# Performance work log

Measured on AMD Instinct MI355X. Metric: run time of the kernel, lower is better.

Reference implementation:

```python
import jax, jax.numpy as jnp
import numpy as np

DIM = 768
B, S = 16, 1024
EPS = 1e-5


def setup_inputs() -> dict:
    key = jax.random.key(0)
    ks = jax.random.split(key, 13)
    std = 1.0 / np.sqrt(DIM)
    inp = {
        "x_A": jax.random.normal(ks[0], (B, S, DIM), jnp.float32),
        "x_B": jax.random.normal(ks[1], (B, S, DIM), jnp.float32),
        "x_C": jax.random.normal(ks[2], (B, S, DIM), jnp.float32),
        "W_q": jax.random.normal(ks[3], (DIM, DIM), jnp.float32) * std,
        "b_q": jax.random.normal(ks[4], (DIM,), jnp.float32) * std,
        "W_k": jax.random.normal(ks[5], (DIM, DIM), jnp.float32) * std,
        "b_k": jax.random.normal(ks[6], (DIM,), jnp.float32) * std,
        "W_v": jax.random.normal(ks[7], (DIM, DIM), jnp.float32) * std,
        "b_v": jax.random.normal(ks[8], (DIM,), jnp.float32) * std,
        "gamma": jnp.ones((DIM,), jnp.float32),
        "beta": jnp.zeros((DIM,), jnp.float32),
        "W_fc": jax.random.normal(ks[9], (DIM, DIM), jnp.float32) * std,
        "b_fc": jax.random.normal(ks[10], (DIM,), jnp.float32) * std,
    }
    return inp


def _linear(x, W, b):
    # torch nn.Linear: x @ W.T + b
    return jnp.einsum('bsd,ed->bse', x, W) + b


def _layernorm(x, gamma, beta):
    mu = jnp.mean(x, axis=-1, keepdims=True)
    var = jnp.mean((x - mu) ** 2, axis=-1, keepdims=True)
    return (x - mu) * jax.lax.rsqrt(var + EPS) * gamma + beta


def reference(x_A, x_B, x_C, W_q, b_q, W_k, b_k, W_v, b_v, gamma, beta, W_fc, b_fc):
    scale = 1.0 / jnp.sqrt(jnp.float32(DIM))
    Q = _linear(x_C, W_q, b_q)
    K_A = _linear(x_A, W_k, b_k)
    K_B = _linear(x_B, W_k, b_k)
    V_A = _linear(x_A, W_v, b_v)
    V_B = _linear(x_B, W_v, b_v)
    attn_A = jax.nn.softmax(jnp.einsum('bqd,bkd->bqk', Q, K_A) * scale, axis=-1)
    attn_B = jax.nn.softmax(jnp.einsum('bqd,bkd->bqk', Q, K_B) * scale, axis=-1)
    interp_A = jnp.einsum('bqk,bkd->bqd', attn_A, V_A)
    interp_B = jnp.einsum('bqk,bkd->bqd', attn_B, V_B)
    h = _layernorm(interp_A + interp_B + x_C, gamma, beta)
    return _linear(h, W_fc, b_fc)
```

## Files before the change

kernel.cpp:

```cpp
#include <hip/hip_runtime.h>

#define DIMV 768
#define BATCH 16
#define SEQ 1024
#define LN_EPS 1e-5f

typedef __attribute__((ext_vector_type(8))) short bf16x8;
typedef __attribute__((ext_vector_type(4))) float f32x4;
typedef unsigned short ushort_t;

__device__ __forceinline__ unsigned short f2bf(float f) {
    unsigned u = __float_as_uint(f);
    u = (u + 0x7FFFu + ((u >> 16) & 1u)) >> 16;
    return (unsigned short)u;
}

__global__ __launch_bounds__(256) void gemm_bf16_nt(
    const ushort_t* __restrict__ A, const ushort_t* __restrict__ B,
    const float* __restrict__ bias, const float* __restrict__ bias2,
    void* __restrict__ Cout, void* __restrict__ Cout2,
    int K, int lda, int ldb, int ldc, float scale, int mode,
    long long sAz, long long sBz, long long sCz)
{
    int bx = blockIdx.x, by = blockIdx.y, bz = blockIdx.z;
    {
        const unsigned Z  = gridDim.z;
        const unsigned nx = gridDim.x, ny = gridDim.y;
        if (Z > 1) {
            const unsigned nxy = nx * ny;
            const unsigned lid = ((unsigned)bz * ny + (unsigned)by) * nx + (unsigned)bx;
            unsigned r;
            if ((Z & 7u) == 0u) {
                const unsigned c  = lid & 7u;
                const unsigned rp = lid >> 3;
                bz = (int)(c + 8u * (rp / nxy));
                r  = rp % nxy;
            } else {
                bz = (int)(lid % Z);
                r  = lid / Z;
            }
            bx = (int)(r % nx);
            by = (int)(r / nx);
        } else {
            const unsigned nwg = nx * ny;
            if ((nwg & 7u) == 0u) {
                const unsigned lid = (unsigned)by * nx + (unsigned)bx;
                const unsigned nl  = (lid & 7u) * (nwg >> 3) + (lid >> 3);
                bx = (int)(nl % nx);
                by = (int)(nl / nx);
            }
        }
    }

    A += (long long)bz * sAz;
    B += (long long)bz * sBz;
    float*    Cf  = (float*)Cout    + ((mode == 0 || mode == 3) ? (long long)bz * sCz : 0);
    ushort_t* Ch  = (ushort_t*)Cout + ((mode == 1 || mode == 2) ? (long long)bz * sCz : 0);
    ushort_t* Ch2 = (ushort_t*)Cout2;

    __shared__ ushort_t As[3][128 * 32];
    __shared__ ushort_t Bs[3][128 * 32];

    const int t    = threadIdx.x;
    const int wave = t >> 6;
    const int lane = t & 63;
    const int quad = lane >> 4;
    const int lr   = lane & 15;
    const int wy   = wave >> 1;
    const int wx   = wave & 1;

    const int m0 = by * 128;
    const int n0 = bx * 128;

    const ushort_t* Abase = A + (long long)m0 * lda;
    const ushort_t* Bbase = B + (long long)n0 * ldb;

    auto issue = [&](int k0, int slot) {
        #pragma unroll
        for (int i = 0; i < 2; ++i) {
            const int idx = t + 256 * i;
            const int r   = idx >> 2;
            const int q   = idx & 3;
            const int c   = (q ^ ((r >> 1) & 3)) * 8;
            __builtin_amdgcn_global_load_lds(
                (const __attribute__((address_space(1))) unsigned int*)(Abase + (long long)r * lda + k0 + c),
                (__attribute__((address_space(3))) unsigned int*)&As[slot][idx * 8], 16, 0, 0);
            __builtin_amdgcn_global_load_lds(
                (const __attribute__((address_space(1))) unsigned int*)(Bbase + (long long)r * ldb + k0 + c),
                (__attribute__((address_space(3))) unsigned int*)&Bs[slot][idx * 8], 16, 0, 0);
        }
    };

    int offA[4], offB[4];
    #pragma unroll
    for (int i = 0; i < 4; ++i) {
        const int rowA = wy * 64 + i * 16 + lr;
        offA[i] = rowA * 32 + ((quad ^ ((rowA >> 1) & 3)) * 8);
        const int rowB = wx * 64 + i * 16 + lr;
        offB[i] = rowB * 32 + ((quad ^ ((rowB >> 1) & 3)) * 8);
    }

    f32x4 acc[4][4] = {};

    const int NK = K >> 5;
    issue(0, 0);
    int cur = 0, nxt = 1;
    for (int ki = 0; ki < NK; ++ki) {
        const int kn = (ki + 1 < NK) ? (ki + 1) << 5 : 0;
        issue(kn, nxt);
        asm volatile("s_waitcnt vmcnt(4)" ::: "memory");
        asm volatile("s_barrier" ::: "memory");

        const ushort_t* as = &As[cur][0];
        const ushort_t* bs = &Bs[cur][0];
        bf16x8 af[4], bfr[4];
        #pragma unroll
        for (int i = 0; i < 4; ++i) af[i]  = *(const bf16x8*)&as[offA[i]];
        #pragma unroll
        for (int j = 0; j < 4; ++j) bfr[j] = *(const bf16x8*)&bs[offB[j]];

        #pragma unroll
        for (int i = 0; i < 4; ++i)
            #pragma unroll
            for (int j = 0; j < 4; ++j)
                acc[i][j] = __builtin_amdgcn_mfma_f32_16x16x32_bf16(
                    af[i], bfr[j], acc[i][j], 0, 0, 0);

        cur = nxt;
        nxt = (nxt == 2) ? 0 : nxt + 1;
    }

    #pragma unroll
    for (int j = 0; j < 4; ++j) {
        const int n = n0 + wx * 64 + j * 16 + lr;
        float bv;
        if (mode == 4) bv = (n < DIMV) ? bias[n] : bias2[n - DIMV];
        else           bv = bias ? bias[n] : 0.0f;
        #pragma unroll
        for (int i = 0; i < 4; ++i) {
            #pragma unroll
            for (int r = 0; r < 4; ++r) {
                const int m = m0 + wy * 64 + i * 16 + quad * 4 + r;
                const float val = acc[i][j][r] * scale + bv;
                if (mode == 0) {
                    Cf[(long long)m * ldc + n] = val;
                } else if (mode == 3) {
                    Cf[(long long)m * ldc + n] += val;
                } else if (mode == 1) {
                    Ch[(long long)m * ldc + n] = f2bf(val);
                } else if (mode == 2) {
                    const int b = m >> 10, s = m & 1023;
                    Ch[(long long)b * (DIMV * SEQ) + (long long)n * SEQ + s] = f2bf(val);
                } else {
                    if (n < DIMV) {
                        Ch[(long long)m * ldc + n] = f2bf(val);
                    } else {
                        const int b = m >> 10, s = m & 1023;
                        Ch2[(long long)b * (DIMV * SEQ) + (long long)(n - DIMV) * SEQ + s] = f2bf(val);
                    }
                }
            }
        }
    }
}

__global__ __launch_bounds__(256) void f32_to_bf16(
    const float* __restrict__ in, ushort_t* __restrict__ out)
{
    const long long i = ((long long)blockIdx.x * 256 + threadIdx.x) * 4;
    float4 v = *reinterpret_cast<const float4*>(in + i);
    ushort4 o;
    o.x = f2bf(v.x); o.y = f2bf(v.y); o.z = f2bf(v.z); o.w = f2bf(v.w);
    *reinterpret_cast<ushort4*>(out + i) = o;
}

__global__ __launch_bounds__(256) void softmax_inplace(float* __restrict__ S)
{
    float* s = S + (long long)blockIdx.x * SEQ;
    const int t = threadIdx.x;
    __shared__ float red[256];

    float4 v = *reinterpret_cast<const float4*>(&s[t * 4]);
    float mx = fmaxf(fmaxf(v.x, v.y), fmaxf(v.z, v.w));
    red[t] = mx;
    __syncthreads();
    for (int st = 128; st > 0; st >>= 1) {
        if (t < st) red[t] = fmaxf(red[t], red[t + st]);
        __syncthreads();
    }
    mx = red[0];
    __syncthreads();

    v.x = __expf(v.x - mx); v.y = __expf(v.y - mx);
    v.z = __expf(v.z - mx); v.w = __expf(v.w - mx);
    red[t] = v.x + v.y + v.z + v.w;
    __syncthreads();
    for (int st = 128; st > 0; st >>= 1) {
        if (t < st) red[t] += red[t + st];
        __syncthreads();
    }
    const float inv = 1.0f / red[0];

    ushort4 o;
    o.x = f2bf(v.x * inv); o.y = f2bf(v.y * inv);
    o.z = f2bf(v.z * inv); o.w = f2bf(v.w * inv);
    *reinterpret_cast<ushort4*>((ushort_t*)s + t * 4) = o;
}

__global__ __launch_bounds__(256) void add_layernorm(
    const float* __restrict__ ACC, const float* __restrict__ xC,
    const float* __restrict__ gamma, const float* __restrict__ beta,
    ushort_t* __restrict__ H)
{
    const long long row = blockIdx.x;
    const float* a = ACC + row * DIMV;
    const float* x = xC  + row * DIMV;
    ushort_t*    h = H   + row * DIMV;
    const int t = threadIdx.x;

    __shared__ float r1[256];
    __shared__ float r2[256];

    float vals[3];
    float s = 0.f, ss = 0.f;
    #pragma unroll
    for (int i = 0; i < 3; ++i) {
        const int j = t + i * 256;
        float v = a[j] + x[j];
        vals[i] = v;
        s += v; ss += v * v;
    }
    r1[t] = s; r2[t] = ss;
    __syncthreads();
    for (int st = 128; st > 0; st >>= 1) {
        if (t < st) { r1[t] += r1[t + st]; r2[t] += r2[t + st]; }
        __syncthreads();
    }
    const float mu  = r1[0] * (1.0f / DIMV);
    const float var = r2[0] * (1.0f / DIMV) - mu * mu;
    const float inv = rsqrtf(var + LN_EPS);

    #pragma unroll
    for (int i = 0; i < 3; ++i) {
        const int j = t + i * 256;
        h[j] = f2bf((vals[i] - mu) * inv * gamma[j] + beta[j]);
    }
}

extern "C" void kernel_launch(void* const* d_in, const int* in_sizes, int n_in,
                              void* d_out, int out_size, void* d_ws, size_t ws_size,
                              hipStream_t stream)
{
    const float* xA    = (const float*)d_in[0];
    const float* xB    = (const float*)d_in[1];
    const float* xC    = (const float*)d_in[2];
    const float* Wq    = (const float*)d_in[3];
    const float* bq    = (const float*)d_in[4];
    const float* Wk    = (const float*)d_in[5];
    const float* bk    = (const float*)d_in[6];
    const float* Wv    = (const float*)d_in[7];
    const float* bv    = (const float*)d_in[8];
    const float* gamma = (const float*)d_in[9];
    const float* beta  = (const float*)d_in[10];
    const float* Wfc   = (const float*)d_in[11];
    const float* bfc   = (const float*)d_in[12];
    float* out = (float*)d_out;

    const long long eW   = (long long)DIMV * DIMV;
    const long long perB = (long long)SEQ * DIMV;
    const long long perP = (long long)SEQ * SEQ;

    const long long wBytes        = 4 * eW * 2;
    const long long perBatchBytes = 14 * perB + 4 * perP;

    long long Cmax = ((long long)ws_size - wBytes) / perBatchBytes;
    if (Cmax > BATCH) Cmax = BATCH;
    if (Cmax < 1)     Cmax = 1;
    const int nChunks = (int)((BATCH + Cmax - 1) / Cmax);
    const int CbStd   = (BATCH + nChunks - 1) / nChunks;

    char* cur = (char*)d_ws;
    ushort_t* Wqb  = (ushort_t*)cur; cur += eW * 2;
    ushort_t* Wkvb = (ushort_t*)cur; cur += 2 * eW * 2;
    ushort_t* Wfcb = (ushort_t*)cur; cur += eW * 2;
    char* chunkBase = cur;

    const float scale = 0.03608439182435161f;

    f32_to_bf16<<<(int)(eW / 1024), 256, 0, stream>>>(Wq,  Wqb);
    f32_to_bf16<<<(int)(eW / 1024), 256, 0, stream>>>(Wk,  Wkvb);
    f32_to_bf16<<<(int)(eW / 1024), 256, 0, stream>>>(Wv,  Wkvb + eW);
    f32_to_bf16<<<(int)(eW / 1024), 256, 0, stream>>>(Wfc, Wfcb);

    for (int b0 = 0; b0 < BATCH; b0 += CbStd) {
        const int Cb = (b0 + CbStd <= BATCH) ? CbStd : (BATCH - b0);
        const long long off = (long long)b0 * perB;

        char* p = chunkBase;
        ushort_t* xABb = (ushort_t*)p;
        float*    ACC  = (float*)p;    p += (long long)Cb * 4 * perB;
        float*    Sf   = (float*)p;
        ushort_t* xCb  = (ushort_t*)p; p += (long long)Cb * 4 * perP;
        ushort_t* Qb   = (ushort_t*)p; p += (long long)Cb * 2 * perB;
        ushort_t* Kb   = (ushort_t*)p; p += (long long)Cb * 4 * perB;
        ushort_t* Vtb  = (ushort_t*)p; p += (long long)Cb * 4 * perB;

        dim3 gq  (DIMV / 128, Cb * (SEQ / 128), 1);
        dim3 gkv (2 * DIMV / 128, 2 * Cb * (SEQ / 128), 1);
        dim3 gsc (SEQ / 128, SEQ / 128, Cb);
        dim3 gpv (DIMV / 128, SEQ / 128, Cb);
        const int gcv = (int)((long long)Cb * perB / 1024);

        f32_to_bf16<<<gcv, 256, 0, stream>>>(xC + off, xCb);
        gemm_bf16_nt<<<gq, 256, 0, stream>>>(xCb, Wqb, bq, nullptr, Qb, nullptr,
            DIMV, DIMV, DIMV, DIMV, 1.f, 1, 0, 0, 0);
        f32_to_bf16<<<gcv, 256, 0, stream>>>(xA + off, xABb);
        f32_to_bf16<<<gcv, 256, 0, stream>>>(xB + off, xABb + (long long)Cb * perB);
        gemm_bf16_nt<<<gkv, 256, 0, stream>>>(xABb, Wkvb, bk, bv, Kb, Vtb,
            DIMV, DIMV, DIMV, DIMV, 1.f, 4, 0, 0, 0);

        gemm_bf16_nt<<<gsc, 256, 0, stream>>>(Qb, Kb, nullptr, nullptr, Sf, nullptr,
            DIMV, DIMV, DIMV, SEQ, scale, 0, perB, perB, perP);
        softmax_inplace<<<Cb * SEQ, 256, 0, stream>>>(Sf);
        gemm_bf16_nt<<<gpv, 256, 0, stream>>>((const ushort_t*)Sf, Vtb, nullptr, nullptr, ACC, nullptr,
            SEQ, 2 * SEQ, SEQ, DIMV, 1.f, 0, 2 * perP, perB, perB);

        gemm_bf16_nt<<<gsc, 256, 0, stream>>>(Qb, Kb + (long long)Cb * perB, nullptr, nullptr, Sf, nullptr,
            DIMV, DIMV, DIMV, SEQ, scale, 0, perB, perB, perP);
        softmax_inplace<<<Cb * SEQ, 256, 0, stream>>>(Sf);
        gemm_bf16_nt<<<gpv, 256, 0, stream>>>((const ushort_t*)Sf, Vtb + (long long)Cb * perB, nullptr, nullptr, ACC, nullptr,
            SEQ, 2 * SEQ, SEQ, DIMV, 1.f, 3, 2 * perP, perB, perB);

        add_layernorm<<<Cb * SEQ, 256, 0, stream>>>(ACC, xC + off, gamma, beta, Qb);

        gemm_bf16_nt<<<gq, 256, 0, stream>>>(Qb, Wfcb, bfc, nullptr, out + off, nullptr,
            DIMV, DIMV, DIMV, DIMV, 1.f, 0, 0, 0, 0);
    }
}
```

Before: 731.9 us.

## Merge A/B attention into single concatenated-key pass and deepen GEMM prefetch to 4 stages

Lays out K for A and B interleaved per batch (and V transposed with 2*SEQ columns), so one score GEMM computes both Q·K_A and Q·K_B. A single softmax kernel normalises each half separately, and one PV GEMM with K=2048 sums both attention outputs. This removes two launches and the read-modify-write accumulate pass. The GEMM mainloop also moves from a 3-slot, 1-ahead prefetch to a 4-slot, 2-ahead prefetch, which uses more LDS and may lower occupancy. The score buffer doubles, which can reduce how many batches fit in one chunk.

```diff
diff --git a/kernel.cpp b/kernel.cpp
--- a/kernel.cpp
+++ b/kernel.cpp
@@ -20,7 +20,7 @@
     const float* __restrict__ bias, const float* __restrict__ bias2,
     void* __restrict__ Cout, void* __restrict__ Cout2,
     int K, int lda, int ldb, int ldc, float scale, int mode,
-    long long sAz, long long sBz, long long sCz)
+    long long sAz, long long sBz, long long sCz, int CbArg)
 {
     int bx = blockIdx.x, by = blockIdx.y, bz = blockIdx.z;
     {
@@ -54,12 +54,12 @@
 
     A += (long long)bz * sAz;
     B += (long long)bz * sBz;
-    float*    Cf  = (float*)Cout    + ((mode == 0 || mode == 3) ? (long long)bz * sCz : 0);
-    ushort_t* Ch  = (ushort_t*)Cout + ((mode == 1 || mode == 2) ? (long long)bz * sCz : 0);
+    float*    Cf  = (float*)Cout    + ((mode == 0) ? (long long)bz * sCz : 0);
+    ushort_t* Ch  = (ushort_t*)Cout + ((mode == 1) ? (long long)bz * sCz : 0);
     ushort_t* Ch2 = (ushort_t*)Cout2;
 
-    __shared__ ushort_t As[3][128 * 32];
-    __shared__ ushort_t Bs[3][128 * 32];
+    __shared__ ushort_t As[4][128 * 32];
+    __shared__ ushort_t Bs[4][128 * 32];
 
     const int t    = threadIdx.x;
     const int wave = t >> 6;
@@ -104,15 +104,15 @@
 
     const int NK = K >> 5;
     issue(0, 0);
-    int cur = 0, nxt = 1;
+    issue(32, 1);
     for (int ki = 0; ki < NK; ++ki) {
-        const int kn = (ki + 1 < NK) ? (ki + 1) << 5 : 0;
-        issue(kn, nxt);
-        asm volatile("s_waitcnt vmcnt(4)" ::: "memory");
+        const int k2 = (ki + 2 < NK) ? (ki + 2) << 5 : (NK - 1) << 5;
+        issue(k2, (ki + 2) & 3);
+        asm volatile("s_waitcnt vmcnt(8)" ::: "memory");
         asm volatile("s_barrier" ::: "memory");
 
-        const ushort_t* as = &As[cur][0];
-        const ushort_t* bs = &Bs[cur][0];
+        const ushort_t* as = &As[ki & 3][0];
+        const ushort_t* bs = &Bs[ki & 3][0];
         bf16x8 af[4], bfr[4];
         #pragma unroll
         for (int i = 0; i < 4; ++i) af[i]  = *(const bf16x8*)&as[offA[i]];
@@ -125,9 +125,6 @@
             for (int j = 0; j < 4; ++j)
                 acc[i][j] = __builtin_amdgcn_mfma_f32_16x16x32_bf16(
                     af[i], bfr[j], acc[i][j], 0, 0, 0);
-
-        cur = nxt;
-        nxt = (nxt == 2) ? 0 : nxt + 1;
     }
 
     #pragma unroll
@@ -144,19 +141,16 @@
                 const float val = acc[i][j][r] * scale + bv;
                 if (mode == 0) {
                     Cf[(long long)m * ldc + n] = val;
-                } else if (mode == 3) {
-                    Cf[(long long)m * ldc + n] += val;
                 } else if (mode == 1) {
                     Ch[(long long)m * ldc + n] = f2bf(val);
-                } else if (mode == 2) {
-                    const int b = m >> 10, s = m & 1023;
-                    Ch[(long long)b * (DIMV * SEQ) + (long long)n * SEQ + s] = f2bf(val);
                 } else {
+                    const int bh = m >> 10, s = m & 1023;
+                    const int hf = (bh >= CbArg) ? 1 : 0;
+                    const int b  = bh - (hf ? CbArg : 0);
                     if (n < DIMV) {
-                        Ch[(long long)m * ldc + n] = f2bf(val);
+                        Ch[(long long)b * (2 * SEQ * DIMV) + (long long)(hf * SEQ + s) * DIMV + n] = f2bf(val);
                     } else {
-                        const int b = m >> 10, s = m & 1023;
-                        Ch2[(long long)b * (DIMV * SEQ) + (long long)(n - DIMV) * SEQ + s] = f2bf(val);
+                        Ch2[(long long)b * (2 * SEQ * DIMV) + (long long)(n - DIMV) * (2 * SEQ) + hf * SEQ + s] = f2bf(val);
                     }
                 }
             }
@@ -174,37 +168,47 @@
     *reinterpret_cast<ushort4*>(out + i) = o;
 }
 
-__global__ __launch_bounds__(256) void softmax_inplace(float* __restrict__ S)
-{
-    float* s = S + (long long)blockIdx.x * SEQ;
-    const int t = threadIdx.x;
+__global__ __launch_bounds__(256) void softmax2_inplace(float* __restrict__ S)
+{
+    float* s = S + (long long)blockIdx.x * (2 * SEQ);
+    const int t  = threadIdx.x;
+    const int hf = t >> 7;
+    const int tt = t & 127;
+    const int base = hf * SEQ + tt * 8;
     __shared__ float red[256];
 
-    float4 v = *reinterpret_cast<const float4*>(&s[t * 4]);
-    float mx = fmaxf(fmaxf(v.x, v.y), fmaxf(v.z, v.w));
+    float4 v0 = *reinterpret_cast<const float4*>(&s[base]);
+    float4 v1 = *reinterpret_cast<const float4*>(&s[base + 4]);
+    float mx = fmaxf(fmaxf(fmaxf(v0.x, v0.y), fmaxf(v0.z, v0.w)),
+                     fmaxf(fmaxf(v1.x, v1.y), fmaxf(v1.z, v1.w)));
     red[t] = mx;
     __syncthreads();
-    for (int st = 128; st > 0; st >>= 1) {
-        if (t < st) red[t] = fmaxf(red[t], red[t + st]);
+    for (int st = 64; st > 0; st >>= 1) {
+        if (tt < st) red[t] = fmaxf(red[t], red[t + st]);
         __syncthreads();
     }
-    mx = red[0];
+    mx = red[hf << 7];
     __syncthreads();
 
-    v.x = __expf(v.x - mx); v.y = __expf(v.y - mx);
-    v.z = __expf(v.z - mx); v.w = __expf(v.w - mx);
-    red[t] = v.x + v.y + v.z + v.w;
+    v0.x = __expf(v0.x - mx); v0.y = __expf(v0.y - mx);
+    v0.z = __expf(v0.z - mx); v0.w = __expf(v0.w - mx);
+    v1.x = __expf(v1.x - mx); v1.y = __expf(v1.y - mx);
+    v1.z = __expf(v1.z - mx); v1.w = __expf(v1.w - mx);
+    red[t] = (v0.x + v0.y + v0.z + v0.w) + (v1.x + v1.y + v1.z + v1.w);
     __syncthreads();
-    for (int st = 128; st > 0; st >>= 1) {
-        if (t < st) red[t] += red[t + st];
+    for (int st = 64; st > 0; st >>= 1) {
+        if (tt < st) red[t] += red[t + st];
         __syncthreads();
     }
-    const float inv = 1.0f / red[0];
-
-    ushort4 o;
-    o.x = f2bf(v.x * inv); o.y = f2bf(v.y * inv);
-    o.z = f2bf(v.z * inv); o.w = f2bf(v.w * inv);
-    *reinterpret_cast<ushort4*>((ushort_t*)s + t * 4) = o;
+    const float inv = 1.0f / red[hf << 7];
+
+    ushort4 o0, o1;
+    o0.x = f2bf(v0.x * inv); o0.y = f2bf(v0.y * inv);
+    o0.z = f2bf(v0.z * inv); o0.w = f2bf(v0.w * inv);
+    o1.x = f2bf(v1.x * inv); o1.y = f2bf(v1.y * inv);
+    o1.z = f2bf(v1.z * inv); o1.w = f2bf(v1.w * inv);
+    *reinterpret_cast<ushort4*>((ushort_t*)s + base)     = o0;
+    *reinterpret_cast<ushort4*>((ushort_t*)s + base + 4) = o1;
 }
 
 __global__ __launch_bounds__(256) void add_layernorm(
@@ -271,7 +275,7 @@
     const long long perP = (long long)SEQ * SEQ;
 
     const long long wBytes        = 4 * eW * 2;
-    const long long perBatchBytes = 14 * perB + 4 * perP;
+    const long long perBatchBytes = 14 * perB + 8 * perP;
 
     long long Cmax = ((long long)ws_size - wBytes) / perBatchBytes;
     if (Cmax > BATCH) Cmax = BATCH;
@@ -300,40 +304,36 @@
         ushort_t* xABb = (ushort_t*)p;
         float*    ACC  = (float*)p;    p += (long long)Cb * 4 * perB;
         float*    Sf   = (float*)p;
-        ushort_t* xCb  = (ushort_t*)p; p += (long long)Cb * 4 * perP;
+        ushort_t* xCb  = (ushort_t*)p; p += (long long)Cb * 8 * perP;
         ushort_t* Qb   = (ushort_t*)p; p += (long long)Cb * 2 * perB;
         ushort_t* Kb   = (ushort_t*)p; p += (long long)Cb * 4 * perB;
         ushort_t* Vtb  = (ushort_t*)p; p += (long long)Cb * 4 * perB;
 
         dim3 gq  (DIMV / 128, Cb * (SEQ / 128), 1);
         dim3 gkv (2 * DIMV / 128, 2 * Cb * (SEQ / 128), 1);
-        dim3 gsc (SEQ / 128, SEQ / 128, Cb);
+        dim3 gsc2(2 * SEQ / 128, SEQ / 128, Cb);
         dim3 gpv (DIMV / 128, SEQ / 128, Cb);
         const int gcv = (int)((long long)Cb * perB / 1024);
 
         f32_to_bf16<<<gcv, 256, 0, stream>>>(xC + off, xCb);
         gemm_bf16_nt<<<gq, 256, 0, stream>>>(xCb, Wqb, bq, nullptr, Qb, nullptr,
-            DIMV, DIMV, DIMV, DIMV, 1.f, 1, 0, 0, 0);
+            DIMV, DIMV, DIMV, DIMV, 1.f, 1, 0, 0, 0, 0);
         f32_to_bf16<<<gcv, 256, 0, stream>>>(xA + off, xABb);
         f32_to_bf16<<<gcv, 256, 0, stream>>>(xB + off, xABb + (long long)Cb * perB);
         gemm_bf16_nt<<<gkv, 256, 0, stream>>>(xABb, Wkvb, bk, bv, Kb, Vtb,
-            DIMV, DIMV, DIMV, DIMV, 1.f, 4, 0, 0, 0);
-
-        gemm_bf16_nt<<<gsc, 256, 0, stream>>>(Qb, Kb, nullptr, nullptr, Sf, nullptr,
-            DIMV, DIMV, DIMV, SEQ, scale, 0, perB, perB, perP);
-        softmax_inplace<<<Cb * SEQ, 256, 0, stream>>>(Sf);
+            DIMV, DIMV, DIMV, DIMV, 1.f, 4, 0, 0, 0, Cb);
+
+        gemm_bf16_nt<<<gsc2, 256, 0, stream>>>(Qb, Kb, nullptr, nullptr, Sf, nullptr,
+            DIMV, DIMV, DIMV, 2 * SEQ, scale, 0, perB, 2 * perB, 2 * perP, 0);
+
+        softmax2_inplace<<<Cb * SEQ, 256, 0, stream>>>(Sf);
+
         gemm_bf16_nt<<<gpv, 256, 0, stream>>>((const ushort_t*)Sf, Vtb, nullptr, nullptr, ACC, nullptr,
-            SEQ, 2 * SEQ, SEQ, DIMV, 1.f, 0, 2 * perP, perB, perB);
-
-        gemm_bf16_nt<<<gsc, 256, 0, stream>>>(Qb, Kb + (long long)Cb * perB, nullptr, nullptr, Sf, nullptr,
-            DIMV, DIMV, DIMV, SEQ, scale, 0, perB, perB, perP);
-        softmax_inplace<<<Cb * SEQ, 256, 0, stream>>>(Sf);
-        gemm_bf16_nt<<<gpv, 256, 0, stream>>>((const ushort_t*)Sf, Vtb + (long long)Cb * perB, nullptr, nullptr, ACC, nullptr,
-            SEQ, 2 * SEQ, SEQ, DIMV, 1.f, 3, 2 * perP, perB, perB);
+            2 * SEQ, 4 * SEQ, 2 * SEQ, DIMV, 1.f, 0, 4 * perP, 2 * perB, perB, 0);
 
         add_layernorm<<<Cb * SEQ, 256, 0, stream>>>(ACC, xC + off, gamma, beta, Qb);
 
         gemm_bf16_nt<<<gq, 256, 0, stream>>>(Qb, Wfcb, bfc, nullptr, out + off, nullptr,
-            DIMV, DIMV, DIMV, DIMV, 1.f, 0, 0, 0, 0);
-    }
-}
+            DIMV, DIMV, DIMV, DIMV, 1.f, 0, 0, 0, 0, 0);
+    }
+}
```

Result: no change. 732.8 us (+0.1%).
